# Kernel optimization log

Hardware: AMD Instinct MI355X
Metric: run time of the kernel (lower is better)

## Reference

```python
import jax, jax.numpy as jnp
import numpy as np

NC = 64
B, H, W = 32, 128, 128


def setup_inputs() -> dict:
    key = jax.random.key(0)
    kx, = jax.random.split(key, 1)
    x = jax.random.normal(kx, (B, NC, H, W), dtype=jnp.float32)
    # params as initialized in the torch module
    exp_param = jnp.eye(NC, dtype=jnp.float32)[:, :, None, None]  # (nc, nc, 1, 1)
    bias = jnp.zeros((NC, 1, 1), dtype=jnp.float32)               # (nc, 1, 1)
    return {"x": x, "exp_param": exp_param, "bias": bias}


def reference(x, exp_param, bias):
    # x: (B, nc, H, W); exp_param: (nc, nc, 1, 1); bias: (nc, 1, 1)
    xr = jax.nn.relu(x) + 0.1  # strictly positive -> log is safe
    # prod_i xr[b,i,h,w] ** E[i,j]  ==  exp( sum_i E[i,j] * log xr[b,i,h,w] )
    # Fused form avoids materializing the (B, nc, nc, H, W) intermediate.
    E = exp_param[:, :, 0, 0]  # (nc_in=i, nc_out=j)
    logx = jnp.log(xr)
    out = jnp.exp(jnp.einsum('bihw,ij->bjhw', logx, E)) + bias  # (B, nc, H, W)
    return out
```

## Files before the change

kernel.cpp:

```cpp
#include <hip/hip_runtime.h>

#define NCH 64
#define HWSZ 16384
#define NPOINTS (32 * HWSZ)
#define TPTS 128
#define NTILES (NPOINTS / TPTS)
#define NBLOCKS 1024
#define TPB 4

typedef __attribute__((ext_vector_type(8))) short bf16x8;
typedef __attribute__((ext_vector_type(4))) float f32x4;

union fragU { bf16x8 v; unsigned int u[4]; };

static __device__ __forceinline__ unsigned int fbits(float f) {
    return __float_as_uint(f);
}
static __device__ __forceinline__ float bfup(unsigned int b) {
    return __uint_as_float(b & 0xFFFF0000u);
}

__global__ __launch_bounds__(256, 2) void fused_log_einsum_exp(
    const float* __restrict__ x,
    const float* __restrict__ E,
    const float* __restrict__ bias,
    float* __restrict__ out)
{
    __shared__ float lx[2][NCH][TPTS];

    const int lane = threadIdx.x & 63;
    const int wv   = threadIdx.x >> 6;
    const int lg   = lane >> 4;
    const int ln   = lane & 15;

    bf16x8 bE[4][2];
    #pragma unroll
    for (int m = 0; m < 4; ++m) {
        #pragma unroll
        for (int kk = 0; kk < 2; ++kk) {
            fragU h;
            #pragma unroll
            for (int w = 0; w < 4; ++w) {
                const int i0 = kk * 32 + lg * 8 + 2 * w;
                const int j  = m * 16 + ln;
                h.u[w] = (fbits(E[(i0 + 1) * NCH + j]) & 0xFFFF0000u)
                       | (fbits(E[i0 * NCH + j]) >> 16);
            }
            bE[m][kk] = h.v;
        }
    }

    float bj[4];
    #pragma unroll
    for (int m = 0; m < 4; ++m) bj[m] = bias[m * 16 + ln];

#define TILE_PB(T) ((size_t)(((T) * TPTS) & ~(HWSZ - 1)) * NCH \
                  + (size_t)(((T) * TPTS) & (HWSZ - 1)))

#define STAGE(BSEL, T) do {                                                    \
    const size_t pb_ = TILE_PB(T);                                             \
    _Pragma("unroll")                                                          \
    for (int n_ = 0; n_ < 8; ++n_) {                                           \
        const int row_   = wv * 16 + 2 * n_;                                   \
        const int plane_ = row_ + (lane >> 5);                                 \
        const int sw_    = ((plane_ >> 3) & 1) << 4;                           \
        const size_t g_  = pb_ + (size_t)plane_ * HWSZ                         \
                         + (size_t)(((lane & 31) * 4) ^ sw_);                  \
        __builtin_amdgcn_global_load_lds(                                      \
            (const __attribute__((address_space(1))) unsigned int*)(x + g_),   \
            (__attribute__((address_space(3))) unsigned int*)&lx[BSEL][row_][0],\
            16, 0, 0);                                                         \
    }                                                                          \
} while (0)

#define COMPUTE(BSEL, T) do {                                                  \
    const size_t po_ = TILE_PB(T);                                             \
    _Pragma("unroll")                                                          \
    for (int sub_ = 0; sub_ < 2; ++sub_) {                                     \
        const int pt_ = wv * 32 + sub_ * 16 + ln;                              \
        fragU ah_[2], al_[2];                                                  \
        _Pragma("unroll")                                                      \
        for (int kk_ = 0; kk_ < 2; ++kk_) {                                    \
            _Pragma("unroll")                                                  \
            for (int w_ = 0; w_ < 4; ++w_) {                                   \
                const int i0_ = kk_ * 32 + lg * 8 + 2 * w_;                    \
                const float v0_ = lx[BSEL][i0_][pt_ ^ (((i0_ >> 3) & 1) << 4)];\
                const float v1_ = lx[BSEL][i0_ + 1]                            \
                                    [pt_ ^ ((((i0_ + 1) >> 3) & 1) << 4)];     \
                const float a0_ = __logf(fmaxf(v0_, 0.0f) + 0.1f);             \
                const float a1_ = __logf(fmaxf(v1_, 0.0f) + 0.1f);             \
                ah_[kk_].u[w_] = (fbits(a1_) & 0xFFFF0000u) | (fbits(a0_) >> 16); \
                const float b0_ = a0_ - bfup(fbits(a0_));                      \
                const float b1_ = a1_ - bfup(fbits(a1_));                      \
                al_[kk_].u[w_] = (fbits(b1_) & 0xFFFF0000u) | (fbits(b0_) >> 16); \
            }                                                                  \
        }                                                                      \
        _Pragma("unroll")                                                      \
        for (int m_ = 0; m_ < 4; ++m_) {                                       \
            f32x4 acc_ = {0.f, 0.f, 0.f, 0.f};                                 \
            _Pragma("unroll")                                                  \
            for (int kk_ = 0; kk_ < 2; ++kk_) {                                \
                acc_ = __builtin_amdgcn_mfma_f32_16x16x32_bf16(                \
                           ah_[kk_].v, bE[m_][kk_], acc_, 0, 0, 0);            \
                acc_ = __builtin_amdgcn_mfma_f32_16x16x32_bf16(                \
                           al_[kk_].v, bE[m_][kk_], acc_, 0, 0, 0);            \
            }                                                                  \
            float4 o_;                                                         \
            o_.x = __expf(acc_[0]) + bj[m_];                                   \
            o_.y = __expf(acc_[1]) + bj[m_];                                   \
            o_.z = __expf(acc_[2]) + bj[m_];                                   \
            o_.w = __expf(acc_[3]) + bj[m_];                                   \
            *reinterpret_cast<float4*>(out + po_                               \
                + (size_t)(m_ * 16 + ln) * HWSZ                                \
                + (size_t)(wv * 32 + sub_ * 16 + lg * 4)) = o_;                \
        }                                                                      \
    }                                                                          \
} while (0)

    STAGE(0, (int)blockIdx.x);
    #pragma unroll
    for (int t = 0; t < TPB; ++t) {
        if (t + 1 < TPB) STAGE((t + 1) & 1, (int)blockIdx.x + (t + 1) * NBLOCKS);
        if (t == 0 || t == TPB - 1) {
            asm volatile("s_waitcnt vmcnt(8)" ::: "memory");
        } else {
            asm volatile("s_waitcnt vmcnt(16)" ::: "memory");
        }
        __builtin_amdgcn_s_barrier();
        __builtin_amdgcn_sched_barrier(0);
        COMPUTE(t & 1, (int)blockIdx.x + t * NBLOCKS);
        if (t + 1 < TPB) {
            __builtin_amdgcn_s_barrier();
            __builtin_amdgcn_sched_barrier(0);
        }
    }

#undef TILE_PB
#undef STAGE
#undef COMPUTE
}

extern "C" void kernel_launch(void* const* d_in, const int* in_sizes, int n_in,
                              void* d_out, int out_size, void* d_ws, size_t ws_size,
                              hipStream_t stream) {
    const float* x    = (const float*)d_in[0];
    const float* E    = (const float*)d_in[1];
    const float* bias = (const float*)d_in[2];
    float* out = (float*)d_out;

    dim3 grid(NBLOCKS), block(256);
    hipLaunchKernelGGL(fused_log_einsum_exp, grid, block, 0, stream,
                       x, E, bias, out);
}
```

Measured before the change: 242.6 us.

## Use 512-thread blocks with half-tile staging pipeline over 512-point tiles

Doubles the block to 8 waves and the tile to 512 points, and splits each tile into two 256-point halves held in a single LDS buffer. Each half is loaded while the other half is computed. The grid shrinks to 512 blocks, each handling two tiles. The goal is fewer blocks, longer contiguous global loads per plane, and overlap of loads with compute. The cost is less latency hiding per wave and a reliance on vmcnt-based waits being correct for the new staging order.

```diff
diff --git a/kernel.cpp b/kernel.cpp
--- a/kernel.cpp
+++ b/kernel.cpp
@@ -3,10 +3,10 @@
 #define NCH 64
 #define HWSZ 16384
 #define NPOINTS (32 * HWSZ)
-#define TPTS 128
+#define TPTS 512
 #define NTILES (NPOINTS / TPTS)
-#define NBLOCKS 1024
-#define TPB 4
+#define NBLK 512
+#define HPTS 256
 
 typedef __attribute__((ext_vector_type(8))) short bf16x8;
 typedef __attribute__((ext_vector_type(4))) float f32x4;
@@ -20,13 +20,13 @@
     return __uint_as_float(b & 0xFFFF0000u);
 }
 
-__global__ __launch_bounds__(256, 2) void fused_log_einsum_exp(
+__global__ __launch_bounds__(512, 2) void fused_log_einsum_exp(
     const float* __restrict__ x,
     const float* __restrict__ E,
     const float* __restrict__ bias,
     float* __restrict__ out)
 {
-    __shared__ float lx[2][NCH][TPTS];
+    __shared__ float lxs[NCH][TPTS];
 
     const int lane = threadIdx.x & 63;
     const int wv   = threadIdx.x >> 6;
@@ -49,7 +49,6 @@
             bE[m][kk] = h.v;
         }
     }
-
     float bj[4];
     #pragma unroll
     for (int m = 0; m < 4; ++m) bj[m] = bias[m * 16 + ln];
@@ -57,36 +56,35 @@
 #define TILE_PB(T) ((size_t)(((T) * TPTS) & ~(HWSZ - 1)) * NCH \
                   + (size_t)(((T) * TPTS) & (HWSZ - 1)))
 
-#define STAGE(BSEL, T) do {                                                    \
+#define STAGE(H, T) do {                                                       \
     const size_t pb_ = TILE_PB(T);                                             \
     _Pragma("unroll")                                                          \
     for (int n_ = 0; n_ < 8; ++n_) {                                           \
-        const int row_   = wv * 16 + 2 * n_;                                   \
-        const int plane_ = row_ + (lane >> 5);                                 \
-        const int sw_    = ((plane_ >> 3) & 1) << 4;                           \
-        const size_t g_  = pb_ + (size_t)plane_ * HWSZ                         \
-                         + (size_t)(((lane & 31) * 4) ^ sw_);                  \
+        const int p_  = wv * 8 + n_;                                           \
+        const int sw_ = ((p_ >> 3) & 1) << 4;                                  \
+        const size_t g_ = pb_ + (size_t)p_ * HWSZ + (H) * HPTS                 \
+                        + (size_t)((lane * 4) ^ sw_);                          \
         __builtin_amdgcn_global_load_lds(                                      \
             (const __attribute__((address_space(1))) unsigned int*)(x + g_),   \
-            (__attribute__((address_space(3))) unsigned int*)&lx[BSEL][row_][0],\
+            (__attribute__((address_space(3))) unsigned int*)&lxs[p_][(H) * HPTS],\
             16, 0, 0);                                                         \
     }                                                                          \
 } while (0)
 
-#define COMPUTE(BSEL, T) do {                                                  \
+#define COMPUTE(H, T) do {                                                     \
     const size_t po_ = TILE_PB(T);                                             \
     _Pragma("unroll")                                                          \
     for (int sub_ = 0; sub_ < 2; ++sub_) {                                     \
-        const int pt_ = wv * 32 + sub_ * 16 + ln;                              \
+        const int pq_ = (H) * HPTS + wv * 32 + sub_ * 16 + ln;                 \
         fragU ah_[2], al_[2];                                                  \
         _Pragma("unroll")                                                      \
         for (int kk_ = 0; kk_ < 2; ++kk_) {                                    \
             _Pragma("unroll")                                                  \
             for (int w_ = 0; w_ < 4; ++w_) {                                   \
                 const int i0_ = kk_ * 32 + lg * 8 + 2 * w_;                    \
-                const float v0_ = lx[BSEL][i0_][pt_ ^ (((i0_ >> 3) & 1) << 4)];\
-                const float v1_ = lx[BSEL][i0_ + 1]                            \
-                                    [pt_ ^ ((((i0_ + 1) >> 3) & 1) << 4)];     \
+                const int sw_ = ((i0_ >> 3) & 1) << 4;     \
+                const float v0_ = lxs[i0_][pq_ ^ sw_];                         \
+                const float v1_ = lxs[i0_ + 1][pq_ ^ sw_];                     \
                 const float a0_ = __logf(fmaxf(v0_, 0.0f) + 0.1f);             \
                 const float a1_ = __logf(fmaxf(v1_, 0.0f) + 0.1f);             \
                 ah_[kk_].u[w_] = (fbits(a1_) & 0xFFFF0000u) | (fbits(a0_) >> 16); \
@@ -112,32 +110,37 @@
             o_.w = __expf(acc_[3]) + bj[m_];                                   \
             *reinterpret_cast<float4*>(out + po_                               \
                 + (size_t)(m_ * 16 + ln) * HWSZ                                \
-                + (size_t)(wv * 32 + sub_ * 16 + lg * 4)) = o_;                \
+                + (size_t)((H) * HPTS + wv * 32 + sub_ * 16 + lg * 4)) = o_;   \
         }                                                                      \
     }                                                                          \
 } while (0)
 
-    STAGE(0, (int)blockIdx.x);
-    #pragma unroll
-    for (int t = 0; t < TPB; ++t) {
-        if (t + 1 < TPB) STAGE((t + 1) & 1, (int)blockIdx.x + (t + 1) * NBLOCKS);
-        if (t == 0 || t == TPB - 1) {
-            asm volatile("s_waitcnt vmcnt(8)" ::: "memory");
-        } else {
-            asm volatile("s_waitcnt vmcnt(16)" ::: "memory");
-        }
-        __builtin_amdgcn_s_barrier();
-        __builtin_amdgcn_sched_barrier(0);
-        COMPUTE(t & 1, (int)blockIdx.x + t * NBLOCKS);
-        if (t + 1 < TPB) {
-            __builtin_amdgcn_s_barrier();
-            __builtin_amdgcn_sched_barrier(0);
-        }
-    }
+#define WAIT8_BARRIER do {                                                     \
+    asm volatile("s_waitcnt vmcnt(8)" ::: "memory");                           \
+    __builtin_amdgcn_s_barrier();                                              \
+    __builtin_amdgcn_sched_barrier(0);                                         \
+} while (0)
+
+    const int t0 = (int)blockIdx.x;
+    const int t1 = t0 + NBLK;
+
+    STAGE(0, t0);
+    STAGE(1, t0);
+    WAIT8_BARRIER;
+    COMPUTE(0, t0);
+    WAIT8_BARRIER;
+    STAGE(0, t1);
+    COMPUTE(1, t0);
+    WAIT8_BARRIER;
+    STAGE(1, t1);
+    COMPUTE(0, t1);
+    WAIT8_BARRIER;
+    COMPUTE(1, t1);
 
 #undef TILE_PB
 #undef STAGE
 #undef COMPUTE
+#undef WAIT8_BARRIER
 }
 
 extern "C" void kernel_launch(void* const* d_in, const int* in_sizes, int n_in,
@@ -148,7 +151,7 @@
     const float* bias = (const float*)d_in[2];
     float* out = (float*)d_out;
 
-    dim3 grid(NBLOCKS), block(256);
+    dim3 grid(NBLK), block(512);
     hipLaunchKernelGGL(fused_log_einsum_exp, grid, block, 0, stream,
                        x, E, bias, out);
 }
```

After: 247.0 us. Within noise of the previous version (+1.8%).
